# Performance work log

Measured on AMD Instinct MI355X. Metric: run time of the kernel, lower is better.

The kernel has to match this reference:

```python
import jax, jax.numpy as jnp
import numpy as np

N_NODES = 50000
N_EDGES = 800000


def _gcn_norm(edge_index, n_nodes):
    # add self loops, compute symmetric normalization coefficients (PyG GCNConv)
    loop = jnp.arange(n_nodes, dtype=edge_index.dtype)
    src = jnp.concatenate([edge_index[0], loop])
    dst = jnp.concatenate([edge_index[1], loop])
    deg = jax.ops.segment_sum(jnp.ones_like(dst, dtype=jnp.float32), dst, num_segments=n_nodes)
    dinv = jnp.where(deg > 0, jax.lax.rsqrt(deg), 0.0)
    coef = dinv[src] * dinv[dst]  # [E + N]
    return src, dst, coef


def _gcn_conv(x, src, dst, coef, W, b, n_nodes):
    h = x @ W                                   # [N, out]
    msg = h[src] * coef[:, None]                # gather + scale
    agg = jax.ops.segment_sum(msg, dst, num_segments=n_nodes)
    return agg + b


def setup_inputs() -> dict:
    key = jax.random.key(0)
    ks = jax.random.split(key, 10)
    d_in, d_hid, d_out = 128, 512, 256
    num_class = [30, 25, 20, 3000]
    inp = {
        "x": jax.random.normal(ks[0], (N_NODES, d_in), dtype=jnp.float32),
        "edge_index": jax.random.randint(ks[1], (2, N_EDGES), 0, N_NODES, dtype=jnp.int64),
        "W1": jax.random.normal(ks[2], (d_in, d_hid), dtype=jnp.float32) / np.sqrt(d_in),
        "b1": jnp.zeros((d_hid,), dtype=jnp.float32),
        "W2": jax.random.normal(ks[3], (d_hid, d_out), dtype=jnp.float32) / np.sqrt(d_hid),
        "b2": jnp.zeros((d_out,), dtype=jnp.float32),
        "Wt": jax.random.normal(ks[4], (d_out, num_class[0]), dtype=jnp.float32) / np.sqrt(d_out),
        "bt": jnp.zeros((num_class[0],), dtype=jnp.float32),
        "Ws": jax.random.normal(ks[5], (d_out, num_class[1]), dtype=jnp.float32) / np.sqrt(d_out),
        "bs": jnp.zeros((num_class[1],), dtype=jnp.float32),
        "Wf": jax.random.normal(ks[6], (d_out, num_class[2]), dtype=jnp.float32) / np.sqrt(d_out),
        "bf": jnp.zeros((num_class[2],), dtype=jnp.float32),
        "Wa": jax.random.normal(ks[7], (d_out, num_class[3]), dtype=jnp.float32) / np.sqrt(d_out),
        "ba": jnp.zeros((num_class[3],), dtype=jnp.float32),
    }
    return inp


def reference(x, edge_index, W1, b1, W2, b2, Wt, bt, Ws, bs, Wf, bf, Wa, ba):
    n = x.shape[0]
    src, dst, coef = _gcn_norm(edge_index, n)
    h = jax.nn.relu(_gcn_conv(x, src, dst, coef, W1, b1, n))
    # dropout is identity at eval time
    g = _gcn_conv(h, src, dst, coef, W2, b2, n)  # graph embedding [N, 256]
    out_type = g @ Wt + bt
    out_school = g @ Ws + bs
    out_time = g @ Wf + bf
    out_author = g @ Wa + ba
    return (out_type, out_school, out_time, out_author)
```

## Files before the change

### kernel.cpp

```cpp
#include <hip/hip_runtime.h>

#define N_NODES 50000
#define N_EDGES 800000

typedef __attribute__((ext_vector_type(8))) short short8;
typedef __attribute__((ext_vector_type(4))) float f32x4;
typedef __attribute__((ext_vector_type(4))) unsigned short u16x4;

__device__ inline unsigned short f2b(float f) {
  union { float f; unsigned int u; } c; c.f = f;
  unsigned int u = c.u;
  u += 0x7FFF + ((u >> 16) & 1);
  return (unsigned short)(u >> 16);
}
__device__ inline float b2f_lo(unsigned int u) {
  union { unsigned int u; float f; } c; c.u = u << 16; return c.f;
}
__device__ inline float b2f_hi(unsigned int u) {
  union { unsigned int u; float f; } c; c.u = u & 0xFFFF0000u; return c.f;
}


__global__ void k_deg(const int* __restrict__ ei, int* __restrict__ deg) {
  int e = blockIdx.x * 256 + threadIdx.x;
  if (e < N_EDGES) atomicAdd(&deg[ei[N_EDGES + e]], 1);
}

__global__ void k_dinv(const int* __restrict__ deg, float* __restrict__ dinv) {
  int n = blockIdx.x * 256 + threadIdx.x;
  if (n < N_NODES) dinv[n] = rsqrtf((float)(deg[n] + 1));
}

__global__ void k_scan(const int* __restrict__ cnt, int* __restrict__ rowptr) {
  __shared__ int wsum[16];
  int tid = threadIdx.x, lane = tid & 63, wv = tid >> 6;
  int carry = 0;
  for (int base = 0; base < N_NODES; base += 1024) {
    int i = base + tid;
    int v = (i < N_NODES) ? cnt[i] : 0;
    int s = v;
#pragma unroll
    for (int off = 1; off < 64; off <<= 1) {
      int u = __shfl_up(s, off, 64);
      if (lane >= off) s += u;
    }
    if (lane == 63) wsum[wv] = s;
    __syncthreads();
    int ws = (lane < 16) ? wsum[lane] : 0;
#pragma unroll
    for (int off = 1; off < 16; off <<= 1) {
      int u = __shfl_up(ws, off, 64);
      if (lane >= off && lane < 16) ws += u;
    }
    int wOff = (wv == 0) ? 0 : __shfl(ws, wv - 1, 64);
    int total = __shfl(ws, 15, 64);
    if (i < N_NODES) rowptr[i] = carry + wOff + (s - v);
    carry += total;
    __syncthreads();
  }
  if (tid == 0) rowptr[N_NODES] = carry;
}

__global__ void k_fill(const int* __restrict__ ei, const int* __restrict__ rowptr,
                       int* __restrict__ cur, int* __restrict__ csr) {
  int e = blockIdx.x * 256 + threadIdx.x;
  if (e < N_EDGES) {
    int d = ei[N_EDGES + e];
    int p = atomicAdd(&cur[d], 1);
    csr[rowptr[d] + p] = ei[e];
  }
}

__global__ void k_cvt(const float* __restrict__ x, unsigned short* __restrict__ xb) {
  int i = blockIdx.x * 256 + threadIdx.x;
  const float4* x4 = (const float4*)x;
  if (i < N_NODES * 128 / 4) {
    float4 v = x4[i];
    ushort4 o; o.x = f2b(v.x); o.y = f2b(v.y); o.z = f2b(v.z); o.w = f2b(v.w);
    ((ushort4*)xb)[i] = o;
  }
}


__global__ void k_packW(const float* __restrict__ W, unsigned short* __restrict__ Bp,
                        int KS, int N) {
  int idx = blockIdx.x * 256 + threadIdx.x;
  int units = ((N + 127) / 128) * KS * 512;
  if (idx >= units) return;
  int grp = idx & 3, col = (idx >> 2) & 127;
  int rest = idx >> 9;
  int s = rest % KS, chunk = rest / KS;
  int gcol = chunk * 128 + col, k0 = s * 32 + grp * 8;
  unsigned short o[8];
#pragma unroll
  for (int j = 0; j < 8; ++j)
    o[j] = (gcol < N) ? f2b(W[(size_t)(k0 + j) * N + gcol]) : 0;
  *(short8*)(Bp + (size_t)idx * 8) = *(short8*)o;
}

__global__ void k_packH(const float* __restrict__ Wt, const float* __restrict__ Ws,
                        const float* __restrict__ Wf, const float* __restrict__ Wa,
                        const float* __restrict__ bt, const float* __restrict__ bs,
                        const float* __restrict__ bfv, const float* __restrict__ ba,
                        unsigned short* __restrict__ Bp, float* __restrict__ bcat) {
  int idx = blockIdx.x * 256 + threadIdx.x;
  const int KS = 8;
  if (idx < 102400) {
    int grp = idx & 3, col = (idx >> 2) & 127;
    int rest = idx >> 9;
    int s = rest % KS, chunk = rest / KS;
    int gcol = chunk * 128 + col, k0 = s * 32 + grp * 8;
    const float* W = Wt; int ld = 30, c = 0;
    bool ok = true;
    if (gcol < 30)                        { W = Wt; ld = 30;   c = gcol; }
    else if (gcol < 55)                   { W = Ws; ld = 25;   c = gcol - 30; }
    else if (gcol < 75)                   { W = Wf; ld = 20;   c = gcol - 55; }
    else if (gcol >= 76 && gcol < 3076)   { W = Wa; ld = 3000; c = gcol - 76; }
    else                                  { ok = false; }
    unsigned short o[8];
#pragma unroll
    for (int j = 0; j < 8; ++j)
      o[j] = ok ? f2b(W[(size_t)(k0 + j) * ld + c]) : 0;
    *(short8*)(Bp + (size_t)idx * 8) = *(short8*)o;
  }
  if (idx < 3200) {
    float v = 0.f;
    if (idx < 30)                      v = bt[idx];
    else if (idx < 55)                 v = bs[idx - 30];
    else if (idx < 75)                 v = bfv[idx - 55];
    else if (idx >= 76 && idx < 3076)  v = ba[idx - 76];
    bcat[idx] = v;
  }
}


__global__ void k_agg1(const unsigned short* __restrict__ xb, const float* __restrict__ dinv,
                       const int* __restrict__ rowptr, const int* __restrict__ csr,
                       unsigned short* __restrict__ A1) {
  int n = blockIdx.x * 4 + (threadIdx.x >> 6);
  if (n >= N_NODES) return;
  int l = threadIdx.x & 63;
  float dn = dinv[n];
  const unsigned int* x2 = (const unsigned int*)xb;
  unsigned int sv = x2[(size_t)n * 64 + l];
  float a0 = b2f_lo(sv) * dn * dn, a1 = b2f_hi(sv) * dn * dn;
  int e = rowptr[n], e1 = rowptr[n + 1];
  for (; e + 4 <= e1; e += 4) {
    int s0 = csr[e], s1 = csr[e + 1], s2 = csr[e + 2], s3 = csr[e + 3];
    float c0 = dinv[s0] * dn, c1 = dinv[s1] * dn, c2 = dinv[s2] * dn, c3 = dinv[s3] * dn;
    unsigned int v0 = x2[(size_t)s0 * 64 + l];
    unsigned int v1 = x2[(size_t)s1 * 64 + l];
    unsigned int v2 = x2[(size_t)s2 * 64 + l];
    unsigned int v3 = x2[(size_t)s3 * 64 + l];
    a0 += b2f_lo(v0) * c0 + b2f_lo(v1) * c1 + b2f_lo(v2) * c2 + b2f_lo(v3) * c3;
    a1 += b2f_hi(v0) * c0 + b2f_hi(v1) * c1 + b2f_hi(v2) * c2 + b2f_hi(v3) * c3;
  }
  for (; e < e1; ++e) {
    int s = csr[e];
    float c = dinv[s] * dn;
    unsigned int v = x2[(size_t)s * 64 + l];
    a0 += b2f_lo(v) * c; a1 += b2f_hi(v) * c;
  }
  unsigned int pk = (unsigned int)f2b(a0) | ((unsigned int)f2b(a1) << 16);
  ((unsigned int*)A1)[(size_t)n * 64 + l] = pk;
}

__global__ void k_agg2(const unsigned short* __restrict__ t, const float* __restrict__ dinv,
                       const int* __restrict__ rowptr, const int* __restrict__ csr,
                       const float* __restrict__ b2, unsigned short* __restrict__ g) {
  int n = blockIdx.x * 4 + (threadIdx.x >> 6);
  if (n >= N_NODES) return;
  int l = threadIdx.x & 63;
  float dn = dinv[n];
  const uint2* t4 = (const uint2*)t;
  uint2 sv = t4[(size_t)n * 64 + l];
  float a0 = b2f_lo(sv.x) * dn * dn, a1 = b2f_hi(sv.x) * dn * dn;
  float a2 = b2f_lo(sv.y) * dn * dn, a3 = b2f_hi(sv.y) * dn * dn;
  int e = rowptr[n], e1 = rowptr[n + 1];
  for (; e + 4 <= e1; e += 4) {
    int s0 = csr[e], s1 = csr[e + 1], s2 = csr[e + 2], s3 = csr[e + 3];
    float c0 = dinv[s0] * dn, c1 = dinv[s1] * dn, c2 = dinv[s2] * dn, c3 = dinv[s3] * dn;
    uint2 v0 = t4[(size_t)s0 * 64 + l];
    uint2 v1 = t4[(size_t)s1 * 64 + l];
    uint2 v2 = t4[(size_t)s2 * 64 + l];
    uint2 v3 = t4[(size_t)s3 * 64 + l];
    a0 += b2f_lo(v0.x) * c0 + b2f_lo(v1.x) * c1 + b2f_lo(v2.x) * c2 + b2f_lo(v3.x) * c3;
    a1 += b2f_hi(v0.x) * c0 + b2f_hi(v1.x) * c1 + b2f_hi(v2.x) * c2 + b2f_hi(v3.x) * c3;
    a2 += b2f_lo(v0.y) * c0 + b2f_lo(v1.y) * c1 + b2f_lo(v2.y) * c2 + b2f_lo(v3.y) * c3;
    a3 += b2f_hi(v0.y) * c0 + b2f_hi(v1.y) * c1 + b2f_hi(v2.y) * c2 + b2f_hi(v3.y) * c3;
  }
  for (; e < e1; ++e) {
    int s = csr[e];
    float c = dinv[s] * dn;
    uint2 v = t4[(size_t)s * 64 + l];
    a0 += b2f_lo(v.x) * c; a1 += b2f_hi(v.x) * c;
    a2 += b2f_lo(v.y) * c; a3 += b2f_hi(v.y) * c;
  }
  int d0 = l * 4;
  a0 += b2[d0]; a1 += b2[d0 + 1]; a2 += b2[d0 + 2]; a3 += b2[d0 + 3];
  ushort4 o; o.x = f2b(a0); o.y = f2b(a1); o.z = f2b(a2); o.w = f2b(a3);
  ((ushort4*)g)[(size_t)n * 64 + l] = o;
}


template <int KSTEPS, int NCHUNKS, int EPI>
__global__ __launch_bounds__(256)
void gemm_c(const unsigned short* __restrict__ A, const unsigned short* __restrict__ Bp,
            const float* __restrict__ bias, void* __restrict__ out, int M, int npanels) {
  __shared__ float lt[32][132];
  const int K = KSTEPS * 32;
  int nwg = npanels * NCHUNKS;
  int orig = blockIdx.x;
  int q = nwg >> 3, r = nwg & 7, xcd = orig & 7;
  int l = (xcd < r ? xcd * (q + 1) : r * (q + 1) + (xcd - r) * q) + (orig >> 3);
  int panel = l / NCHUNKS, chunk = l - panel * NCHUNKS;
  int tid = threadIdx.x, lane = tid & 63, w = tid >> 6;
  int ln = lane & 15, grp = lane >> 4;
  int row0 = panel * 64;

  int arow[4];
#pragma unroll
  for (int m = 0; m < 4; ++m) {
    int gr = row0 + m * 16 + ln;
    arow[m] = gr < M ? gr : M - 1;
  }

  f32x4 acc[4][2];
  f32x4 z = {0.f, 0.f, 0.f, 0.f};
#pragma unroll
  for (int m = 0; m < 4; ++m) { acc[m][0] = z; acc[m][1] = z; }

#pragma unroll 4
  for (int s = 0; s < KSTEPS; ++s) {
    short8 bfr[2];
#pragma unroll
    for (int n = 0; n < 2; ++n) {
      size_t unit = ((size_t)(chunk * KSTEPS + s) * 128 + (w * 32 + n * 16 + ln)) * 4 + grp;
      bfr[n] = *(const short8*)(Bp + unit * 8);
    }
    short8 am[4];
#pragma unroll
    for (int m = 0; m < 4; ++m)
      am[m] = *(const short8*)(A + (size_t)arow[m] * K + s * 32 + grp * 8);
#pragma unroll
    for (int m = 0; m < 4; ++m)
#pragma unroll
      for (int n = 0; n < 2; ++n)
        acc[m][n] = __builtin_amdgcn_mfma_f32_16x16x32_bf16(am[m], bfr[n], acc[m][n], 0, 0, 0);
  }

  int c0 = chunk * 128;
  float bv[2];
#pragma unroll
  for (int n = 0; n < 2; ++n)
    bv[n] = (EPI == 1) ? 0.f : bias[c0 + w * 32 + n * 16 + ln];

#pragma unroll
  for (int half = 0; half < 2; ++half) {
    if (half) __syncthreads();
#pragma unroll
    for (int n = 0; n < 2; ++n) {
#pragma unroll
      for (int mm = 0; mm < 2; ++mm) {
        int m = half * 2 + mm;
#pragma unroll
        for (int rr = 0; rr < 4; ++rr) {
          float v = acc[m][n][rr] + bv[n];
          if (EPI == 0) v = v > 0.f ? v : 0.f;
          lt[mm * 16 + grp * 4 + rr][w * 32 + n * 16 + ln] = v;
        }
      }
    }
    __syncthreads();

    int col4 = tid & 31, rowi = tid >> 5;
#pragma unroll
    for (int rr = 0; rr < 4; ++rr) {
      int rw = rr * 8 + rowi;
      int grow = row0 + half * 32 + rw;
      if (grow >= M) continue;
      f32x4 v = *(const f32x4*)&lt[rw][col4 * 4];
      if (EPI == 2) {
        int gcn0 = c0 + col4 * 4;
        float* o = (float*)out;
        if (gcn0 >= 76 && gcn0 + 4 <= 3076) {
          __builtin_nontemporal_store(v, (f32x4*)(o + 3750000ull + (size_t)grow * 3000 + (gcn0 - 76)));
        } else {
#pragma unroll
          for (int j = 0; j < 4; ++j) {
            int gcn = gcn0 + j;
            if (gcn >= 3076) continue;
            size_t offo;
            if (gcn < 30)      offo = (size_t)grow * 30 + gcn;
            else if (gcn < 55) offo = 1500000ull + (size_t)grow * 25 + (gcn - 30);
            else if (gcn < 75) offo = 2750000ull + (size_t)grow * 20 + (gcn - 55);
            else if (gcn == 75) continue;
            else               offo = 3750000ull + (size_t)grow * 3000 + (gcn - 76);
            o[offo] = v[j];
          }
        }
      } else {
        const int NOUT = NCHUNKS * 128;
        u16x4 b;
        b[0] = f2b(v[0]); b[1] = f2b(v[1]); b[2] = f2b(v[2]); b[3] = f2b(v[3]);
        *(u16x4*)((unsigned short*)out + (size_t)grow * NOUT + c0 + col4 * 4) = b;
      }
    }
  }
}


extern "C" void kernel_launch(void* const* d_in, const int* in_sizes, int n_in,
                              void* d_out, int out_size, void* d_ws, size_t ws_size,
                              hipStream_t stream) {
  const float* x  = (const float*)d_in[0];
  const int* ei   = (const int*)d_in[1];
  const float* W1 = (const float*)d_in[2];
  const float* b1 = (const float*)d_in[3];
  const float* W2 = (const float*)d_in[4];
  const float* b2 = (const float*)d_in[5];
  const float* Wt = (const float*)d_in[6];
  const float* bt = (const float*)d_in[7];
  const float* Ws = (const float*)d_in[8];
  const float* bs = (const float*)d_in[9];
  const float* Wf = (const float*)d_in[10];
  const float* bf_ = (const float*)d_in[11];
  const float* Wa = (const float*)d_in[12];
  const float* ba = (const float*)d_in[13];

  char* ws = (char*)d_ws;
  size_t off = 0;
  auto alloc = [&](size_t bytes) {
    void* p = ws + off;
    off = (off + bytes + 255) & ~(size_t)255;
    return p;
  };
  int* deg    = (int*)alloc(N_NODES * 4);
  int* cur    = (int*)alloc(N_NODES * 4);
  float* dinv = (float*)alloc(N_NODES * 4);
  int* rowptr = (int*)alloc((N_NODES + 1) * 4);
  int* csr    = (int*)alloc((size_t)N_EDGES * 4);
  unsigned short* xb = (unsigned short*)alloc((size_t)N_NODES * 128 * 2);
  unsigned short* A1 = (unsigned short*)alloc((size_t)N_NODES * 128 * 2);
  unsigned short* h  = (unsigned short*)alloc((size_t)N_NODES * 512 * 2);
  unsigned short* t  = (unsigned short*)alloc((size_t)N_NODES * 256 * 2);
  unsigned short* g  = h;
  unsigned short* Bp0 = (unsigned short*)alloc((size_t)512 * 128 * 2);
  unsigned short* Bp1 = (unsigned short*)alloc((size_t)256 * 512 * 2);
  unsigned short* BpH = (unsigned short*)alloc((size_t)3200 * 256 * 2);
  float* bcat = (float*)alloc(3200 * 4);

  const int NP = (N_NODES + 63) / 64;

  hipMemsetAsync(deg, 0, N_NODES * 4, stream);
  hipMemsetAsync(cur, 0, N_NODES * 4, stream);
  k_deg<<<(N_EDGES + 255) / 256, 256, 0, stream>>>(ei, deg);
  k_dinv<<<(N_NODES + 255) / 256, 256, 0, stream>>>(deg, dinv);
  k_scan<<<1, 1024, 0, stream>>>(deg, rowptr);
  k_fill<<<(N_EDGES + 255) / 256, 256, 0, stream>>>(ei, rowptr, cur, csr);
  k_cvt<<<(N_NODES * 128 / 4 + 255) / 256, 256, 0, stream>>>(x, xb);
  k_packW<<<(512 * 128 / 8 + 255) / 256, 256, 0, stream>>>(W1, Bp0, 4, 512);
  k_packW<<<(256 * 512 / 8 + 255) / 256, 256, 0, stream>>>(W2, Bp1, 16, 256);
  k_packH<<<(102400 + 255) / 256, 256, 0, stream>>>(Wt, Ws, Wf, Wa, bt, bs, bf_, ba, BpH, bcat);
  k_agg1<<<(N_NODES + 3) / 4, 256, 0, stream>>>(xb, dinv, rowptr, csr, A1);
  gemm_c<4, 4, 0><<<NP * 4, 256, 0, stream>>>(A1, Bp0, b1, h, N_NODES, NP);
  gemm_c<16, 2, 1><<<NP * 2, 256, 0, stream>>>(h, Bp1, nullptr, t, N_NODES, NP);
  k_agg2<<<(N_NODES + 3) / 4, 256, 0, stream>>>(t, dinv, rowptr, csr, b2, g);
  gemm_c<8, 25, 2><<<NP * 25, 256, 0, stream>>>(g, BpH, bcat, d_out, N_NODES, NP);
}
```

Baseline: 737.3 us.

## Fuse prep kernels, fold dinv into scan, unroll gathers by 8, single-pass epilogue

```diff
diff --git a/kernel.cpp b/kernel.cpp
--- a/kernel.cpp
+++ b/kernel.cpp
@@ -26,18 +26,15 @@
   if (e < N_EDGES) atomicAdd(&deg[ei[N_EDGES + e]], 1);
 }
 
-__global__ void k_dinv(const int* __restrict__ deg, float* __restrict__ dinv) {
-  int n = blockIdx.x * 256 + threadIdx.x;
-  if (n < N_NODES) dinv[n] = rsqrtf((float)(deg[n] + 1));
-}
-
-__global__ void k_scan(const int* __restrict__ cnt, int* __restrict__ rowptr) {
+__global__ void k_scan(const int* __restrict__ cnt, int* __restrict__ rowptr,
+                       float* __restrict__ dinv) {
   __shared__ int wsum[16];
   int tid = threadIdx.x, lane = tid & 63, wv = tid >> 6;
   int carry = 0;
   for (int base = 0; base < N_NODES; base += 1024) {
     int i = base + tid;
     int v = (i < N_NODES) ? cnt[i] : 0;
+    if (i < N_NODES) dinv[i] = rsqrtf((float)(v + 1));
     int s = v;
 #pragma unroll
     for (int off = 1; off < 64; off <<= 1) {
@@ -71,41 +68,56 @@
   }
 }
 
-__global__ void k_cvt(const float* __restrict__ x, unsigned short* __restrict__ xb) {
-  int i = blockIdx.x * 256 + threadIdx.x;
-  const float4* x4 = (const float4*)x;
-  if (i < N_NODES * 128 / 4) {
-    float4 v = x4[i];
+
+#define CVT_UNITS (N_NODES * 128 / 4)
+#define PW1_UNITS (4 * 4 * 512)
+#define PW2_UNITS (2 * 16 * 512)
+#define PH_UNITS  102400
+
+__global__ void k_prep(const float* __restrict__ x, unsigned short* __restrict__ xb,
+                       const float* __restrict__ W1, unsigned short* __restrict__ Bp0,
+                       const float* __restrict__ W2, unsigned short* __restrict__ Bp1,
+                       const float* __restrict__ Wt, const float* __restrict__ Ws,
+                       const float* __restrict__ Wf, const float* __restrict__ Wa,
+                       const float* __restrict__ bt, const float* __restrict__ bs,
+                       const float* __restrict__ bfv, const float* __restrict__ ba,
+                       unsigned short* __restrict__ BpH, float* __restrict__ bcat) {
+  int idx = blockIdx.x * 256 + threadIdx.x;
+  if (idx < CVT_UNITS) {
+    float4 v = ((const float4*)x)[idx];
     ushort4 o; o.x = f2b(v.x); o.y = f2b(v.y); o.z = f2b(v.z); o.w = f2b(v.w);
-    ((ushort4*)xb)[i] = o;
-  }
-}
-
-
-__global__ void k_packW(const float* __restrict__ W, unsigned short* __restrict__ Bp,
-                        int KS, int N) {
-  int idx = blockIdx.x * 256 + threadIdx.x;
-  int units = ((N + 127) / 128) * KS * 512;
-  if (idx >= units) return;
-  int grp = idx & 3, col = (idx >> 2) & 127;
-  int rest = idx >> 9;
-  int s = rest % KS, chunk = rest / KS;
-  int gcol = chunk * 128 + col, k0 = s * 32 + grp * 8;
-  unsigned short o[8];
-#pragma unroll
-  for (int j = 0; j < 8; ++j)
-    o[j] = (gcol < N) ? f2b(W[(size_t)(k0 + j) * N + gcol]) : 0;
-  *(short8*)(Bp + (size_t)idx * 8) = *(short8*)o;
-}
-
-__global__ void k_packH(const float* __restrict__ Wt, const float* __restrict__ Ws,
-                        const float* __restrict__ Wf, const float* __restrict__ Wa,
-                        const float* __restrict__ bt, const float* __restrict__ bs,
-                        const float* __restrict__ bfv, const float* __restrict__ ba,
-                        unsigned short* __restrict__ Bp, float* __restrict__ bcat) {
-  int idx = blockIdx.x * 256 + threadIdx.x;
-  const int KS = 8;
-  if (idx < 102400) {
+    ((ushort4*)xb)[idx] = o;
+    return;
+  }
+  idx -= CVT_UNITS;
+  if (idx < PW1_UNITS) {
+    const int KS = 4, N = 512;
+    int grp = idx & 3, col = (idx >> 2) & 127;
+    int rest = idx >> 9;
+    int s = rest % KS, chunk = rest / KS;
+    int gcol = chunk * 128 + col, k0 = s * 32 + grp * 8;
+    unsigned short o[8];
+#pragma unroll
+    for (int j = 0; j < 8; ++j) o[j] = f2b(W1[(size_t)(k0 + j) * N + gcol]);
+    *(short8*)(Bp0 + (size_t)idx * 8) = *(short8*)o;
+    return;
+  }
+  idx -= PW1_UNITS;
+  if (idx < PW2_UNITS) {
+    const int KS = 16, N = 256;
+    int grp = idx & 3, col = (idx >> 2) & 127;
+    int rest = idx >> 9;
+    int s = rest % KS, chunk = rest / KS;
+    int gcol = chunk * 128 + col, k0 = s * 32 + grp * 8;
+    unsigned short o[8];
+#pragma unroll
+    for (int j = 0; j < 8; ++j) o[j] = f2b(W2[(size_t)(k0 + j) * N + gcol]);
+    *(short8*)(Bp1 + (size_t)idx * 8) = *(short8*)o;
+    return;
+  }
+  idx -= PW2_UNITS;
+  if (idx < PH_UNITS) {
+    const int KS = 8;
     int grp = idx & 3, col = (idx >> 2) & 127;
     int rest = idx >> 9;
     int s = rest % KS, chunk = rest / KS;
@@ -121,15 +133,15 @@
 #pragma unroll
     for (int j = 0; j < 8; ++j)
       o[j] = ok ? f2b(W[(size_t)(k0 + j) * ld + c]) : 0;
-    *(short8*)(Bp + (size_t)idx * 8) = *(short8*)o;
-  }
-  if (idx < 3200) {
-    float v = 0.f;
-    if (idx < 30)                      v = bt[idx];
-    else if (idx < 55)                 v = bs[idx - 30];
-    else if (idx < 75)                 v = bfv[idx - 55];
-    else if (idx >= 76 && idx < 3076)  v = ba[idx - 76];
-    bcat[idx] = v;
+    *(short8*)(BpH + (size_t)idx * 8) = *(short8*)o;
+    if (idx < 3200) {
+      float v = 0.f;
+      if (idx < 30)                      v = bt[idx];
+      else if (idx < 55)                 v = bs[idx - 30];
+      else if (idx < 75)                 v = bfv[idx - 55];
+      else if (idx >= 76 && idx < 3076)  v = ba[idx - 76];
+      bcat[idx] = v;
+    }
   }
 }
 
@@ -145,6 +157,17 @@
   unsigned int sv = x2[(size_t)n * 64 + l];
   float a0 = b2f_lo(sv) * dn * dn, a1 = b2f_hi(sv) * dn * dn;
   int e = rowptr[n], e1 = rowptr[n + 1];
+  for (; e + 8 <= e1; e += 8) {
+    int si[8]; float cf[8]; unsigned int v[8];
+#pragma unroll
+    for (int j = 0; j < 8; ++j) si[j] = csr[e + j];
+#pragma unroll
+    for (int j = 0; j < 8; ++j) cf[j] = dinv[si[j]] * dn;
+#pragma unroll
+    for (int j = 0; j < 8; ++j) v[j] = x2[(size_t)si[j] * 64 + l];
+#pragma unroll
+    for (int j = 0; j < 8; ++j) { a0 += b2f_lo(v[j]) * cf[j]; a1 += b2f_hi(v[j]) * cf[j]; }
+  }
   for (; e + 4 <= e1; e += 4) {
     int s0 = csr[e], s1 = csr[e + 1], s2 = csr[e + 2], s3 = csr[e + 3];
     float c0 = dinv[s0] * dn, c1 = dinv[s1] * dn, c2 = dinv[s2] * dn, c3 = dinv[s3] * dn;
@@ -177,6 +200,20 @@
   float a0 = b2f_lo(sv.x) * dn * dn, a1 = b2f_hi(sv.x) * dn * dn;
   float a2 = b2f_lo(sv.y) * dn * dn, a3 = b2f_hi(sv.y) * dn * dn;
   int e = rowptr[n], e1 = rowptr[n + 1];
+  for (; e + 8 <= e1; e += 8) {
+    int si[8]; float cf[8]; uint2 v[8];
+#pragma unroll
+    for (int j = 0; j < 8; ++j) si[j] = csr[e + j];
+#pragma unroll
+    for (int j = 0; j < 8; ++j) cf[j] = dinv[si[j]] * dn;
+#pragma unroll
+    for (int j = 0; j < 8; ++j) v[j] = t4[(size_t)si[j] * 64 + l];
+#pragma unroll
+    for (int j = 0; j < 8; ++j) {
+      a0 += b2f_lo(v[j].x) * cf[j]; a1 += b2f_hi(v[j].x) * cf[j];
+      a2 += b2f_lo(v[j].y) * cf[j]; a3 += b2f_hi(v[j].y) * cf[j];
+    }
+  }
   for (; e + 4 <= e1; e += 4) {
     int s0 = csr[e], s1 = csr[e + 1], s2 = csr[e + 2], s3 = csr[e + 3];
     float c0 = dinv[s0] * dn, c1 = dinv[s1] * dn, c2 = dinv[s2] * dn, c3 = dinv[s3] * dn;
@@ -207,7 +244,7 @@
 __global__ __launch_bounds__(256)
 void gemm_c(const unsigned short* __restrict__ A, const unsigned short* __restrict__ Bp,
             const float* __restrict__ bias, void* __restrict__ out, int M, int npanels) {
-  __shared__ float lt[32][132];
+  __shared__ float lt[64][132];
   const int K = KSTEPS * 32;
   int nwg = npanels * NCHUNKS;
   int orig = blockIdx.x;
@@ -250,61 +287,52 @@
   }
 
   int c0 = chunk * 128;
-  float bv[2];
-#pragma unroll
-  for (int n = 0; n < 2; ++n)
-    bv[n] = (EPI == 1) ? 0.f : bias[c0 + w * 32 + n * 16 + ln];
-
-#pragma unroll
-  for (int half = 0; half < 2; ++half) {
-    if (half) __syncthreads();
-#pragma unroll
-    for (int n = 0; n < 2; ++n) {
-#pragma unroll
-      for (int mm = 0; mm < 2; ++mm) {
-        int m = half * 2 + mm;
-#pragma unroll
-        for (int rr = 0; rr < 4; ++rr) {
-          float v = acc[m][n][rr] + bv[n];
-          if (EPI == 0) v = v > 0.f ? v : 0.f;
-          lt[mm * 16 + grp * 4 + rr][w * 32 + n * 16 + ln] = v;
+#pragma unroll
+  for (int n = 0; n < 2; ++n) {
+    int gcn = c0 + w * 32 + n * 16 + ln;
+    float bv = (EPI == 1) ? 0.f : bias[gcn];
+#pragma unroll
+    for (int m = 0; m < 4; ++m)
+#pragma unroll
+      for (int rr = 0; rr < 4; ++rr) {
+        float v = acc[m][n][rr] + bv;
+        if (EPI == 0) v = v > 0.f ? v : 0.f;
+        lt[m * 16 + grp * 4 + rr][w * 32 + n * 16 + ln] = v;
+      }
+  }
+  __syncthreads();
+
+  int col4 = tid & 31, rowi = tid >> 5;
+#pragma unroll
+  for (int rr = 0; rr < 8; ++rr) {
+    int rw = rr * 8 + rowi;
+    int grow = row0 + rw;
+    if (grow >= M) continue;
+    f32x4 v = *(const f32x4*)&lt[rw][col4 * 4];
+    if (EPI == 2) {
+      int gcn0 = c0 + col4 * 4;
+      float* o = (float*)out;
+      if (gcn0 >= 76 && gcn0 + 4 <= 3076) {
+        __builtin_nontemporal_store(v, (f32x4*)(o + 3750000ull + (size_t)grow * 3000 + (gcn0 - 76)));
+      } else {
+#pragma unroll
+        for (int j = 0; j < 4; ++j) {
+          int gcn = gcn0 + j;
+          if (gcn >= 3076) continue;
+          size_t offo;
+          if (gcn < 30)      offo = (size_t)grow * 30 + gcn;
+          else if (gcn < 55) offo = 1500000ull + (size_t)grow * 25 + (gcn - 30);
+          else if (gcn < 75) offo = 2750000ull + (size_t)grow * 20 + (gcn - 55);
+          else if (gcn == 75) continue;
+          else               offo = 3750000ull + (size_t)grow * 3000 + (gcn - 76);
+          o[offo] = v[j];
         }
       }
-    }
-    __syncthreads();
-
-    int col4 = tid & 31, rowi = tid >> 5;
-#pragma unroll
-    for (int rr = 0; rr < 4; ++rr) {
-      int rw = rr * 8 + rowi;
-      int grow = row0 + half * 32 + rw;
-      if (grow >= M) continue;
-      f32x4 v = *(const f32x4*)&lt[rw][col4 * 4];
-      if (EPI == 2) {
-        int gcn0 = c0 + col4 * 4;
-        float* o = (float*)out;
-        if (gcn0 >= 76 && gcn0 + 4 <= 3076) {
-          __builtin_nontemporal_store(v, (f32x4*)(o + 3750000ull + (size_t)grow * 3000 + (gcn0 - 76)));
-        } else {
-#pragma unroll
-          for (int j = 0; j < 4; ++j) {
-            int gcn = gcn0 + j;
-            if (gcn >= 3076) continue;
-            size_t offo;
-            if (gcn < 30)      offo = (size_t)grow * 30 + gcn;
-            else if (gcn < 55) offo = 1500000ull + (size_t)grow * 25 + (gcn - 30);
-            else if (gcn < 75) offo = 2750000ull + (size_t)grow * 20 + (gcn - 55);
-            else if (gcn == 75) continue;
-            else               offo = 3750000ull + (size_t)grow * 3000 + (gcn - 76);
-            o[offo] = v[j];
-          }
-        }
-      } else {
-        const int NOUT = NCHUNKS * 128;
-        u16x4 b;
-        b[0] = f2b(v[0]); b[1] = f2b(v[1]); b[2] = f2b(v[2]); b[3] = f2b(v[3]);
-        *(u16x4*)((unsigned short*)out + (size_t)grow * NOUT + c0 + col4 * 4) = b;
-      }
+    } else {
+      const int NOUT = NCHUNKS * 128;
+      u16x4 b;
+      b[0] = f2b(v[0]); b[1] = f2b(v[1]); b[2] = f2b(v[2]); b[3] = f2b(v[3]);
+      *(u16x4*)((unsigned short*)out + (size_t)grow * NOUT + c0 + col4 * 4) = b;
     }
   }
 }
@@ -351,17 +379,15 @@
   float* bcat = (float*)alloc(3200 * 4);
 
   const int NP = (N_NODES + 63) / 64;
+  const int PREP_UNITS = CVT_UNITS + PW1_UNITS + PW2_UNITS + PH_UNITS;
 
   hipMemsetAsync(deg, 0, N_NODES * 4, stream);
   hipMemsetAsync(cur, 0, N_NODES * 4, stream);
   k_deg<<<(N_EDGES + 255) / 256, 256, 0, stream>>>(ei, deg);
-  k_dinv<<<(N_NODES + 255) / 256, 256, 0, stream>>>(deg, dinv);
-  k_scan<<<1, 1024, 0, stream>>>(deg, rowptr);
+  k_scan<<<1, 1024, 0, stream>>>(deg, rowptr, dinv);
   k_fill<<<(N_EDGES + 255) / 256, 256, 0, stream>>>(ei, rowptr, cur, csr);
-  k_cvt<<<(N_NODES * 128 / 4 + 255) / 256, 256, 0, stream>>>(x, xb);
-  k_packW<<<(512 * 128 / 8 + 255) / 256, 256, 0, stream>>>(W1, Bp0, 4, 512);
-  k_packW<<<(256 * 512 / 8 + 255) / 256, 256, 0, stream>>>(W2, Bp1, 16, 256);
-  k_packH<<<(102400 + 255) / 256, 256, 0, stream>>>(Wt, Ws, Wf, Wa, bt, bs, bf_, ba, BpH, bcat);
+  k_prep<<<(PREP_UNITS + 255) / 256, 256, 0, stream>>>(x, xb, W1, Bp0, W2, Bp1,
+      Wt, Ws, Wf, Wa, bt, bs, bf_, ba, BpH, bcat);
   k_agg1<<<(N_NODES + 3) / 4, 256, 0, stream>>>(xb, dinv, rowptr, csr, A1);
   gemm_c<4, 4, 0><<<NP * 4, 256, 0, stream>>>(A1, Bp0, b1, h, N_NODES, NP);
   gemm_c<16, 2, 1><<<NP * 2, 256, 0, stream>>>(h, Bp1, nullptr, t, N_NODES, NP);
```

After: 715.0 us. -3.0%, faster.
